# Kernel optimization log

Measured on AMD Instinct MI355X. Metric: run time of the kernel, lower is better.

## Reference

```python
import jax, jax.numpy as jnp
import numpy as np

B, T, D = 2, 2048, 1024
H, DK, DV, NH = 8, 128, 256, 2  # heads, key dim, value dim (expand_v=2), num_householder
CONV = 4
INTER = 2816
EPS = 1e-6


def rmsnorm(x, w):
    return x * jax.lax.rsqrt(jnp.mean(x * x, -1, keepdims=True) + EPS) * w


def l2norm(x):
    return x * jax.lax.rsqrt(jnp.sum(x * x, -1, keepdims=True) + 1e-6)


def causal_conv_silu(x, w):
    # depthwise causal conv1d with silu activation; x: [B,T,C], w: [C,K]
    K = w.shape[1]
    xp = jnp.pad(x, ((0, 0), (K - 1, 0), (0, 0)))
    y = sum(xp[:, i:i + x.shape[1], :] * w[:, i] for i in range(K))
    return jax.nn.silu(y)


def setup_inputs():
    key = jax.random.key(0)
    ks = jax.random.split(key, 16)
    s = 0.02
    return {
        "hidden_states": jax.random.normal(ks[0], (B, T, D), jnp.float32),
        "attn_norm_w": jnp.ones((D,), jnp.float32),
        "Wq": jax.random.normal(ks[1], (D, H * DK), jnp.float32) * s,
        "Wk": jax.random.normal(ks[2], (D, NH * H * DK), jnp.float32) * s,
        "Wv": jax.random.normal(ks[3], (D, NH * H * DV), jnp.float32) * s,
        "Wb": jax.random.normal(ks[4], (D, H * NH), jnp.float32) * s,
        "Wa": jax.random.normal(ks[5], (D, H), jnp.float32) * s,
        "A_log": jnp.log(jax.random.uniform(ks[6], (H,), jnp.float32, 1.0, 16.0)),
        "dt_bias": jax.random.normal(ks[7], (H,), jnp.float32) * 0.5,
        "conv_q_w": jax.random.normal(ks[8], (H * DK, CONV), jnp.float32) * 0.5,
        "conv_k_w": jax.random.normal(ks[9], (NH * H * DK, CONV), jnp.float32) * 0.5,
        "conv_v_w": jax.random.normal(ks[10], (NH * H * DV, CONV), jnp.float32) * 0.5,
        "Wg": jax.random.normal(ks[11], (D, H * DV), jnp.float32) * s,
        "o_norm_w": jnp.ones((DV,), jnp.float32),
        "Wo": jax.random.normal(ks[12], (H * DV, D), jnp.float32) * s,
        "mlp_norm_w": jnp.ones((D,), jnp.float32),
        "Wgate": jax.random.normal(ks[13], (D, 2 * INTER), jnp.float32) * s,
        "Wdown": jax.random.normal(ks[14], (INTER, D), jnp.float32) * s,
    }


def reference(hidden_states, attn_norm_w, Wq, Wk, Wv, Wb, Wa, A_log, dt_bias,
              conv_q_w, conv_k_w, conv_v_w, Wg, o_norm_w, Wo,
              mlp_norm_w, Wgate, Wdown):
    residual = hidden_states
    x = rmsnorm(hidden_states, attn_norm_w)

    # projections + short conv + silu, then L2-normalized q/k (gated delta rule)
    q = l2norm(causal_conv_silu(x @ Wq, conv_q_w).reshape(B, T, H, DK))
    k = l2norm(causal_conv_silu(x @ Wk, conv_k_w).reshape(B, T, NH, H, DK))
    v = causal_conv_silu(x @ Wv, conv_v_w).reshape(B, T, NH, H, DV)
    beta = jax.nn.sigmoid(x @ Wb).reshape(B, T, H, NH)
    g = -jnp.exp(A_log) * jax.nn.softplus(x @ Wa + dt_bias)  # [B,T,H] log-decay

    def step(S, inp):
        q_t, k_t, v_t, b_t, g_t = inp
        # forget gate applied once per token, then NH Householder delta-rule updates
        S = S * jnp.exp(g_t)[..., None, None]  # S: [B,H,DK,DV]
        for j in range(NH):
            kj, vj, bj = k_t[:, j], v_t[:, j], b_t[..., j]
            kS = jnp.einsum('bhk,bhkv->bhv', kj, S)
            S = S + bj[..., None, None] * jnp.einsum('bhk,bhv->bhkv', kj, vj - kS)
        o_t = jnp.einsum('bhk,bhkv->bhv', q_t, S)
        return S, o_t

    S0 = jnp.zeros((B, H, DK, DV), x.dtype)
    xs = (jnp.swapaxes(q, 0, 1), jnp.swapaxes(k, 0, 1), jnp.swapaxes(v, 0, 1),
          jnp.swapaxes(beta, 0, 1), jnp.swapaxes(g, 0, 1))
    _, o = jax.lax.scan(step, S0, xs)  # [T,B,H,DV]
    o = jnp.swapaxes(o, 0, 1)

    # gated RMSNorm output gate + output projection
    gate = (x @ Wg).reshape(B, T, H, DV)
    o = rmsnorm(o, o_norm_w) * jax.nn.silu(gate)
    hidden = residual + o.reshape(B, T, H * DV) @ Wo

    # GatedMLP (swiglu)
    y = rmsnorm(hidden, mlp_norm_w)
    gate_m, up = jnp.split(y @ Wgate, 2, -1)
    return hidden + (jax.nn.silu(gate_m) * up) @ Wdown
```

## Files before the change

kernel.cpp:

```cpp
#include <hip/hip_runtime.h>
#include <hip/hip_bf16.h>
#include <math.h>

#define Bq 2
#define Tq 2048
#define Dq 1024
#define Hq 8
#define DKq 128
#define DVq 256
#define NHq 2
#define BTq (Bq*Tq)
#define INTERq 2816

typedef __hip_bfloat16 bf16;
typedef short bfv8 __attribute__((ext_vector_type(8)));
typedef float f32v4 __attribute__((ext_vector_type(4)));

__device__ __forceinline__ float b2f(bf16 v){ return __bfloat162float(v); }
__device__ __forceinline__ bf16 f2b(float v){ return __float2bfloat16(v); }

__device__ __forceinline__ int is_f32(const unsigned* magic){ return magic[0] == 0x3F800000u; }

__device__ __forceinline__ float ldin(const void* p, int f32, size_t i){
  return f32 ? ((const float*)p)[i] : b2f(((const bf16*)p)[i]);
}

__device__ __forceinline__ float block_reduce_sum(float v, float* red){
  #pragma unroll
  for (int off = 32; off > 0; off >>= 1) v += __shfl_down(v, off, 64);
  int lane = threadIdx.x & 63, wid = threadIdx.x >> 6;
  if (lane == 0) red[wid] = v;
  __syncthreads();
  int nw = (blockDim.x + 63) >> 6;
  float tot = 0.f;
  for (int i = 0; i < nw; i++) tot += red[i];
  return tot;
}

__global__ __launch_bounds__(256) void rmsnorm_kernel(const void* __restrict__ in, int in_mode,
    const void* __restrict__ w, const unsigned* __restrict__ magic,
    bf16* __restrict__ out){
  __shared__ float red[4];
  int f32 = is_f32(magic);
  int inf32 = in_mode ? 1 : f32;
  size_t row = blockIdx.x;
  float xv[4];
  float ss = 0.f;
  #pragma unroll
  for (int j = 0; j < 4; j++){
    int i = threadIdx.x + j*256;
    float v = ldin(in, inf32, row*Dq + i);
    xv[j] = v; ss += v*v;
  }
  float tot = block_reduce_sum(ss, red);
  float sc = rsqrtf(tot / (float)Dq + 1e-6f);
  #pragma unroll
  for (int j = 0; j < 4; j++){
    int i = threadIdx.x + j*256;
    out[row*Dq + i] = f2b(xv[j] * sc * ldin(w, f32, i));
  }
}

__global__ __launch_bounds__(256) void wsplit_kernel(
    const void* __restrict__ W, const unsigned* __restrict__ magic,
    bf16* __restrict__ hi, bf16* __restrict__ lo, int K, int N){
  __shared__ float tile[32][33];
  int f32 = is_f32(magic);
  int n0 = blockIdx.x * 32, k0 = blockIdx.y * 32;
  int tx = threadIdx.x & 31, ty = threadIdx.x >> 5;
  #pragma unroll
  for (int r = 0; r < 4; r++){
    int kr = ty + r*8;
    tile[kr][tx] = ldin(W, f32, (size_t)(k0 + kr)*N + n0 + tx);
  }
  __syncthreads();
  #pragma unroll
  for (int r = 0; r < 4; r++){
    int nr = ty + r*8;
    float v = tile[tx][nr];
    bf16 h = f2b(v);
    size_t idx = (size_t)(n0 + nr)*K + k0 + tx;
    hi[idx] = h;
    if (f32) lo[idx] = f2b(v - b2f(h));
  }
}

__global__ __launch_bounds__(256) void gemm_mfma_kernel(
    const bf16* __restrict__ A, const bf16* __restrict__ WThi, const bf16* __restrict__ WTlo,
    const unsigned* __restrict__ magic,
    const void* __restrict__ res, int res_mode,
    void* __restrict__ out, int out_mode,
    int M, int N, int K){
  int f32 = is_f32(magic);
  int tid = threadIdx.x;
  int lane = tid & 63, w = tid >> 6;
  int wm = w >> 1, wn = w & 1;
  int l15 = lane & 15, quad = lane >> 4;
  size_t bm = (size_t)blockIdx.x * 128, bn = (size_t)blockIdx.y * 128;

  f32v4 acc[4][4];
  #pragma unroll
  for (int mt = 0; mt < 4; mt++)
    #pragma unroll
    for (int nt = 0; nt < 4; nt++) acc[mt][nt] = 0.f;

  const bf16* Ab = A    + (bm + wm*64 + l15)*(size_t)K + quad*8;
  const bf16* Bh = WThi + (bn + wn*64 + l15)*(size_t)K + quad*8;
  const bf16* Bl = WTlo + (bn + wn*64 + l15)*(size_t)K + quad*8;

  if (f32){
    for (int k0 = 0; k0 < K; k0 += 32){
      bfv8 a[4];
      #pragma unroll
      for (int mt = 0; mt < 4; mt++)
        a[mt] = *(const bfv8*)(Ab + (size_t)mt*16*K + k0);
      #pragma unroll
      for (int nt = 0; nt < 4; nt++){
        bfv8 bh = *(const bfv8*)(Bh + (size_t)nt*16*K + k0);
        bfv8 bl = *(const bfv8*)(Bl + (size_t)nt*16*K + k0);
        #pragma unroll
        for (int mt = 0; mt < 4; mt++){
          acc[mt][nt] = __builtin_amdgcn_mfma_f32_16x16x32_bf16(a[mt], bh, acc[mt][nt], 0, 0, 0);
          acc[mt][nt] = __builtin_amdgcn_mfma_f32_16x16x32_bf16(a[mt], bl, acc[mt][nt], 0, 0, 0);
        }
      }
    }
  } else {
    for (int k0 = 0; k0 < K; k0 += 32){
      bfv8 a[4];
      #pragma unroll
      for (int mt = 0; mt < 4; mt++)
        a[mt] = *(const bfv8*)(Ab + (size_t)mt*16*K + k0);
      #pragma unroll
      for (int nt = 0; nt < 4; nt++){
        bfv8 bh = *(const bfv8*)(Bh + (size_t)nt*16*K + k0);
        #pragma unroll
        for (int mt = 0; mt < 4; mt++)
          acc[mt][nt] = __builtin_amdgcn_mfma_f32_16x16x32_bf16(a[mt], bh, acc[mt][nt], 0, 0, 0);
      }
    }
  }
  #pragma unroll
  for (int mt = 0; mt < 4; mt++)
    #pragma unroll
    for (int nt = 0; nt < 4; nt++)
      #pragma unroll
      for (int r = 0; r < 4; r++){
        size_t row = bm + wm*64 + mt*16 + quad*4 + r;
        size_t col = bn + wn*64 + nt*16 + l15;
        float v = acc[mt][nt][r];
        if (res_mode == 1) v += ldin(res, f32, row*N + col);
        else if (res_mode == 2) v += ((const float*)res)[row*N + col];
        if (out_mode == 0) ((float*)out)[row*N + col] = v;
        else if (out_mode == 1) ((bf16*)out)[row*N + col] = f2b(v);
        else { if (f32) ((float*)out)[row*N + col] = v; else ((bf16*)out)[row*N + col] = f2b(v); }
      }
}

__global__ __launch_bounds__(256) void betag_kernel(
    const bf16* __restrict__ x, const void* __restrict__ Wb, const void* __restrict__ Wa,
    const void* __restrict__ A_log, const void* __restrict__ dt_bias,
    const unsigned* __restrict__ magic,
    float* __restrict__ beta, float* __restrict__ g){
  __shared__ float xs[Dq];
  int f32 = is_f32(magic);
  size_t bt = blockIdx.x;
  for (int i = threadIdx.x; i < Dq; i += 256) xs[i] = b2f(x[bt*Dq + i]);
  __syncthreads();
  int n = threadIdx.x;
  if (n < 16){
    float a = 0.f;
    for (int i = 0; i < Dq; i++) a = fmaf(xs[i], ldin(Wb, f32, (size_t)i*16 + n), a);
    int h = n >> 1, j = n & 1;
    beta[(bt*Hq + h)*NHq + j] = 1.f / (1.f + expf(-a));
  } else if (n < 24){
    int h = n - 16;
    float a = 0.f;
    for (int i = 0; i < Dq; i++) a = fmaf(xs[i], ldin(Wa, f32, (size_t)i*Hq + h), a);
    a += ldin(dt_bias, f32, h);
    float sp = (a > 20.f) ? a : log1pf(expf(a));
    g[bt*Hq + h] = -expf(ldin(A_log, f32, h)) * sp;
  }
}

__global__ __launch_bounds__(128) void conv_silu_kernel(
    const bf16* __restrict__ in, const void* __restrict__ w,
    const unsigned* __restrict__ magic,
    float* __restrict__ out, int C){
  __shared__ float red[2];
  int f32 = is_f32(magic);
  int bt = blockIdx.x;
  int t = bt & (Tq - 1);
  int c = blockIdx.y * 128 + threadIdx.x;
  float acc = 0.f;
  #pragma unroll
  for (int i = 0; i < 4; i++){
    int tt = t - 3 + i;
    if (tt >= 0) acc = fmaf(b2f(in[(size_t)(bt - 3 + i)*C + c]), ldin(w, f32, (size_t)c*4 + i), acc);
  }
  float y = acc / (1.f + expf(-acc));
  float tot = block_reduce_sum(y*y, red);
  y *= rsqrtf(tot + 1e-6f);
  out[(size_t)bt*C + c] = y;
}

#define DPP_ADD(x, ctrl) ((x) + __int_as_float(__builtin_amdgcn_update_dpp( \
    0, __float_as_int(x), (ctrl), 0xF, 0xF, true)))
#define KRED(p) { p = DPP_ADD(p, 0x128); p = DPP_ADD(p, 0x124); \
                  p = DPP_ADD(p, 0x122); p = DPP_ADD(p, 0x121); }

__global__ __launch_bounds__(64, 1) void scan_kernel(
    const float* __restrict__ qn,
    const float* __restrict__ kn,
    const bf16*  __restrict__ vpre,
    const void* __restrict__ conv_v, const unsigned* __restrict__ magic,
    const float* __restrict__ beta,
    const float* __restrict__ g,
    float* __restrict__ o){
  int f32 = is_f32(magic);
  int bh = blockIdx.x;
  int b = bh >> 3, h = bh & 7;
  int lane = threadIdx.x;
  int kg = lane & 15;
  int vloc = lane >> 4;
  int vv = blockIdx.y * 4 + vloc;
  int c0 = (h << 8) + vv;
  int c1 = ((Hq + h) << 8) + vv;
  float wv00 = ldin(conv_v, f32, (size_t)c0*4 + 0);
  float wv01 = ldin(conv_v, f32, (size_t)c0*4 + 1);
  float wv02 = ldin(conv_v, f32, (size_t)c0*4 + 2);
  float wv03 = ldin(conv_v, f32, (size_t)c0*4 + 3);
  float wv10 = ldin(conv_v, f32, (size_t)c1*4 + 0);
  float wv11 = ldin(conv_v, f32, (size_t)c1*4 + 1);
  float wv12 = ldin(conv_v, f32, (size_t)c1*4 + 2);
  float wv13 = ldin(conv_v, f32, (size_t)c1*4 + 3);
  const size_t base = (size_t)b * Tq;
  const float* knh = kn + base*2048 + h*DKq + kg*8;
  const float* qnh = qn + (base*Hq + h)*(size_t)DKq + kg*8;
  const bf16*  vph = vpre + base*4096;
  const float* gh  = g + base*Hq + h;
  const float2* bph = (const float2*)(beta + (base*Hq + h)*(size_t)NHq);
  float* oh = o + (base*Hq + h)*(size_t)DVq + vv;

  float4 S0 = {0,0,0,0}, S1 = {0,0,0,0};
#define SDOT(Ka, Kb, p) { \
    float e0 = fmaf(Ka.x, S0.x, Ka.y * S0.y); \
    float e1 = fmaf(Ka.z, S0.z, Ka.w * S0.w); \
    float e2 = fmaf(Kb.x, S1.x, Kb.y * S1.y); \
    float e3 = fmaf(Kb.z, S1.z, Kb.w * S1.w); \
    p = (e0 + e1) + (e2 + e3); }
#define SUPD(Ka, Kb, d) { \
    S0.x = fmaf(Ka.x, d, S0.x); S0.y = fmaf(Ka.y, d, S0.y); \
    S0.z = fmaf(Ka.z, d, S0.z); S0.w = fmaf(Ka.w, d, S0.w); \
    S1.x = fmaf(Kb.x, d, S1.x); S1.y = fmaf(Kb.y, d, S1.y); \
    S1.z = fmaf(Kb.z, d, S1.z); S1.w = fmaf(Kb.w, d, S1.w); }

  float r0a = 0.f, r1a = 0.f, r2a = 0.f;
  float r0b = 0.f, r1b = 0.f, r2b = 0.f;

  float4 A0E = *(const float4*)(knh);
  float4 A1E = *(const float4*)(knh + 4);
  float4 B0E = *(const float4*)(knh + 1024);
  float4 B1E = *(const float4*)(knh + 1028);
  float4 Q0E = *(const float4*)(qnh);
  float4 Q1E = *(const float4*)(qnh + 4);
  float4 A0O = *(const float4*)(knh + 2048);
  float4 A1O = *(const float4*)(knh + 2052);
  float4 B0O = *(const float4*)(knh + 3072);
  float4 B1O = *(const float4*)(knh + 3076);
  float4 Q0O = *(const float4*)(qnh + 1024);
  float4 Q1O = *(const float4*)(qnh + 1028);
  float  gE  = gh[0],   gO  = gh[8];
  float2 beE = bph[0],  beO = bph[8];
  float vaE = b2f(vph[c0]),        vbE = b2f(vph[c1]);
  float vaO = b2f(vph[4096 + c0]), vbO = b2f(vph[4096 + c1]);

#define STEP(A0,A1,B0,B1,Q0,Q1, gS, beS, vaS, vbS, t, tp) { \
    float eg = __expf(gS); \
    gS = gh[(tp)*8]; \
    S0.x *= eg; S0.y *= eg; S0.z *= eg; S0.w *= eg; \
    S1.x *= eg; S1.y *= eg; S1.z *= eg; S1.w *= eg; \
     \
    { float p; SDOT(A0, A1, p) \
      KRED(p) \
      float vacc = fmaf(r0a, wv00, fmaf(r1a, wv01, fmaf(r2a, wv02, vaS*wv03))); \
      float vj = vacc * __builtin_amdgcn_rcpf(1.f + __expf(-vacc)); \
      float delta = beS.x * (vj - p); \
      SUPD(A0, A1, delta) \
      A0 = *(const float4*)(knh + (tp)*2048); \
      A1 = *(const float4*)(knh + (tp)*2048 + 4); \
      r0a = r1a; r1a = r2a; r2a = vaS; \
      vaS = b2f(vph[(tp)*4096 + c0]); } \
     \
    { float p; SDOT(B0, B1, p) \
      KRED(p) \
      float vacc = fmaf(r0b, wv10, fmaf(r1b, wv11, fmaf(r2b, wv12, vbS*wv13))); \
      float vj = vacc * __builtin_amdgcn_rcpf(1.f + __expf(-vacc)); \
      float delta = beS.y * (vj - p); \
      SUPD(B0, B1, delta) \
      B0 = *(const float4*)(knh + (tp)*2048 + 1024); \
      B1 = *(const float4*)(knh + (tp)*2048 + 1028); \
      r0b = r1b; r1b = r2b; r2b = vbS; \
      vbS = b2f(vph[(tp)*4096 + c1]); } \
    beS = bph[(tp)*8]; \
     \
     \
    { float p; SDOT(Q0, Q1, p) \
      KRED(p) \
      oh[(t)*2048] = p; \
      Q0 = *(const float4*)(qnh + (tp)*1024); \
      Q1 = *(const float4*)(qnh + (tp)*1024 + 4); } \
    __builtin_amdgcn_sched_barrier(0); }

  for (int t = 0; t < Tq; t += 2){
    STEP(A0E,A1E,B0E,B1E,Q0E,Q1E, gE,beE,vaE,vbE, t,   t+2)
    STEP(A0O,A1O,B0O,B1O,Q0O,Q1O, gO,beO,vaO,vbO, t+1, t+3)
  }
#undef STEP
#undef SDOT
#undef SUPD
}

__global__ __launch_bounds__(256) void gate_o_kernel(
    const float* __restrict__ o, const void* __restrict__ onw,
    const unsigned* __restrict__ magic,
    const bf16* __restrict__ gate, bf16* __restrict__ og){
  __shared__ float red[4];
  int f32 = is_f32(magic);
  size_t bth = blockIdx.x;
  int dv = threadIdx.x;
  float v = o[bth*DVq + dv];
  float tot = block_reduce_sum(v*v, red);
  float sc = rsqrtf(tot / (float)DVq + 1e-6f);
  float gt = b2f(gate[bth*DVq + dv]);
  float silu = gt / (1.f + expf(-gt));
  og[bth*DVq + dv] = f2b(v * sc * ldin(onw, f32, dv) * silu);
}

__global__ __launch_bounds__(256) void silumul_kernel(
    const bf16* __restrict__ gu, bf16* __restrict__ mid, int n){
  int i = blockIdx.x * 256 + threadIdx.x;
  if (i >= n) return;
  int bt = i / INTERq, c = i % INTERq;
  float gm = b2f(gu[(size_t)bt*2*INTERq + c]);
  float up = b2f(gu[(size_t)bt*2*INTERq + INTERq + c]);
  mid[i] = f2b(gm / (1.f + expf(-gm)) * up);
}

extern "C" void kernel_launch(void* const* d_in, const int* in_sizes, int n_in,
                              void* d_out, int out_size, void* d_ws, size_t ws_size,
                              hipStream_t stream){
  const void* hs      = d_in[0];
  const unsigned* magic = (const unsigned*)d_in[1];
  const void* attn_nw = d_in[1];
  const void* Wq      = d_in[2];
  const void* Wk      = d_in[3];
  const void* Wv      = d_in[4];
  const void* Wb      = d_in[5];
  const void* Wa      = d_in[6];
  const void* A_log   = d_in[7];
  const void* dt_bias = d_in[8];
  const void* conv_q  = d_in[9];
  const void* conv_k  = d_in[10];
  const void* conv_v  = d_in[11];
  const void* Wg      = d_in[12];
  const void* o_nw    = d_in[13];
  const void* Wo      = d_in[14];
  const void* mlp_nw  = d_in[15];
  const void* Wgate   = d_in[16];
  const void* Wdown   = d_in[17];

  char* ws = (char*)d_ws;
  const size_t MB = (size_t)1 << 20;
  size_t X     = 0;
  size_t QPRE  = 8*MB;
  size_t KPRE  = 16*MB;
  size_t VPRE  = 32*MB;
  size_t GATE  = 64*MB;
  size_t QN    = 80*MB;
  size_t KN    = 96*MB;
  size_t HID   = 128*MB;
  size_t BETA  = 144*MB;
  size_t Gb    = 144*MB + 512*1024;
  size_t O      = 0;
  size_t OG     = QN;
  size_t Y      = KN;
  size_t GATEUP = 0;
  size_t MID    = 44*MB;
  size_t W0 = 145*MB;
  size_t WTQh = W0 +  0*MB, WTQl = W0 +  2*MB;
  size_t WTKh = W0 +  4*MB, WTKl = W0 +  8*MB;
  size_t WTVh = W0 + 12*MB, WTVl = W0 + 20*MB;
  size_t WTGh = W0 + 28*MB, WTGl = W0 + 32*MB;
  size_t WTOh = W0 + 36*MB, WTOl = W0 + 40*MB;
  size_t WTUh = W0 + 44*MB, WTUl = W0 + 56*MB;
  size_t WTDh = W0 + 68*MB, WTDl = W0 + 74*MB;
  (void)ws_size; (void)in_sizes; (void)n_in; (void)out_size;

  wsplit_kernel<<<dim3(1024/32, 1024/32), 256, 0, stream>>>(Wq,    magic, (bf16*)(ws+WTQh), (bf16*)(ws+WTQl), 1024, 1024);
  wsplit_kernel<<<dim3(2048/32, 1024/32), 256, 0, stream>>>(Wk,    magic, (bf16*)(ws+WTKh), (bf16*)(ws+WTKl), 1024, 2048);
  wsplit_kernel<<<dim3(4096/32, 1024/32), 256, 0, stream>>>(Wv,    magic, (bf16*)(ws+WTVh), (bf16*)(ws+WTVl), 1024, 4096);
  wsplit_kernel<<<dim3(2048/32, 1024/32), 256, 0, stream>>>(Wg,    magic, (bf16*)(ws+WTGh), (bf16*)(ws+WTGl), 1024, 2048);
  wsplit_kernel<<<dim3(1024/32, 2048/32), 256, 0, stream>>>(Wo,    magic, (bf16*)(ws+WTOh), (bf16*)(ws+WTOl), 2048, 1024);
  wsplit_kernel<<<dim3(5632/32, 1024/32), 256, 0, stream>>>(Wgate, magic, (bf16*)(ws+WTUh), (bf16*)(ws+WTUl), 1024, 5632);
  wsplit_kernel<<<dim3(1024/32, 2816/32), 256, 0, stream>>>(Wdown, magic, (bf16*)(ws+WTDh), (bf16*)(ws+WTDl), 2816, 1024);

  rmsnorm_kernel<<<BTq, 256, 0, stream>>>(hs, 0, attn_nw, magic, (bf16*)(ws+X));

  gemm_mfma_kernel<<<dim3(32,  8), 256, 0, stream>>>((bf16*)(ws+X), (bf16*)(ws+WTQh), (bf16*)(ws+WTQl), magic, nullptr, 0, ws+QPRE, 1, BTq, 1024, 1024);
  gemm_mfma_kernel<<<dim3(32, 16), 256, 0, stream>>>((bf16*)(ws+X), (bf16*)(ws+WTKh), (bf16*)(ws+WTKl), magic, nullptr, 0, ws+KPRE, 1, BTq, 2048, 1024);
  gemm_mfma_kernel<<<dim3(32, 32), 256, 0, stream>>>((bf16*)(ws+X), (bf16*)(ws+WTVh), (bf16*)(ws+WTVl), magic, nullptr, 0, ws+VPRE, 1, BTq, 4096, 1024);
  gemm_mfma_kernel<<<dim3(32, 16), 256, 0, stream>>>((bf16*)(ws+X), (bf16*)(ws+WTGh), (bf16*)(ws+WTGl), magic, nullptr, 0, ws+GATE, 1, BTq, 2048, 1024);
  betag_kernel<<<BTq, 256, 0, stream>>>((bf16*)(ws+X), Wb, Wa, A_log, dt_bias, magic, (float*)(ws+BETA), (float*)(ws+Gb));

  conv_silu_kernel<<<dim3(BTq, 1024/128), 128, 0, stream>>>((bf16*)(ws+QPRE), conv_q, magic, (float*)(ws+QN), 1024);
  conv_silu_kernel<<<dim3(BTq, 2048/128), 128, 0, stream>>>((bf16*)(ws+KPRE), conv_k, magic, (float*)(ws+KN), 2048);

  scan_kernel<<<dim3(Bq*Hq, DVq/4), 64, 0, stream>>>(
      (const float*)(ws+QN), (const float*)(ws+KN), (const bf16*)(ws+VPRE),
      conv_v, magic, (const float*)(ws+BETA), (const float*)(ws+Gb), (float*)(ws+O));

  gate_o_kernel<<<BTq*Hq, 256, 0, stream>>>((const float*)(ws+O), o_nw, magic, (const bf16*)(ws+GATE), (bf16*)(ws+OG));

  gemm_mfma_kernel<<<dim3(32, 8), 256, 0, stream>>>((bf16*)(ws+OG), (bf16*)(ws+WTOh), (bf16*)(ws+WTOl), magic, hs, 1, ws+HID, 0, BTq, 1024, 2048);

  rmsnorm_kernel<<<BTq, 256, 0, stream>>>(ws+HID, 1, mlp_nw, magic, (bf16*)(ws+Y));

  gemm_mfma_kernel<<<dim3(32, 44), 256, 0, stream>>>((bf16*)(ws+Y), (bf16*)(ws+WTUh), (bf16*)(ws+WTUl), magic, nullptr, 0, ws+GATEUP, 1, BTq, 5632, 1024);

  int nmid = BTq * INTERq;
  silumul_kernel<<<(nmid + 255)/256, 256, 0, stream>>>((const bf16*)(ws+GATEUP), (bf16*)(ws+MID), nmid);

  gemm_mfma_kernel<<<dim3(32, 8), 256, 0, stream>>>((bf16*)(ws+MID), (bf16*)(ws+WTDh), (bf16*)(ws+WTDl), magic, ws+HID, 2, d_out, 2, BTq, 1024, 2816);
}
```

Measured before the change: 2.652 ms.

## Hoist v conv+silu and decay exp out of scan; parallelize beta/g reduction

Moves the causal conv + SiLU on v out of the serial scan into a separate parallel kernel that writes bf16, and precomputes exp(g) in the beta/g kernel so the scan only multiplies. The beta/g kernel now spreads each dot product over a full wavefront with a shuffle reduction instead of one thread per output. The scan's output store is also limited to one lane per 16-lane group instead of all lanes. This shortens the latency-bound per-token critical path, at the cost of an extra kernel launch and an extra bf16 write and read of v.

```diff
diff --git a/kernel.cpp b/kernel.cpp
--- a/kernel.cpp
+++ b/kernel.cpp
@@ -161,25 +161,44 @@
     const bf16* __restrict__ x, const void* __restrict__ Wb, const void* __restrict__ Wa,
     const void* __restrict__ A_log, const void* __restrict__ dt_bias,
     const unsigned* __restrict__ magic,
-    float* __restrict__ beta, float* __restrict__ g){
+    float* __restrict__ beta, float* __restrict__ eg){
   __shared__ float xs[Dq];
   int f32 = is_f32(magic);
   size_t bt = blockIdx.x;
   for (int i = threadIdx.x; i < Dq; i += 256) xs[i] = b2f(x[bt*Dq + i]);
   __syncthreads();
-  int n = threadIdx.x;
-  if (n < 16){
+  int wv = threadIdx.x >> 6, lane = threadIdx.x & 63;
+  #pragma unroll
+  for (int r = 0; r < 6; r++){
+    int n = wv*6 + r;
     float a = 0.f;
-    for (int i = 0; i < Dq; i++) a = fmaf(xs[i], ldin(Wb, f32, (size_t)i*16 + n), a);
-    int h = n >> 1, j = n & 1;
-    beta[(bt*Hq + h)*NHq + j] = 1.f / (1.f + expf(-a));
-  } else if (n < 24){
-    int h = n - 16;
-    float a = 0.f;
-    for (int i = 0; i < Dq; i++) a = fmaf(xs[i], ldin(Wa, f32, (size_t)i*Hq + h), a);
-    a += ldin(dt_bias, f32, h);
-    float sp = (a > 20.f) ? a : log1pf(expf(a));
-    g[bt*Hq + h] = -expf(ldin(A_log, f32, h)) * sp;
+    if (n < 16){
+      #pragma unroll
+      for (int e = 0; e < 16; e++){
+        int i = lane + 64*e;
+        a = fmaf(xs[i], ldin(Wb, f32, (size_t)i*16 + n), a);
+      }
+    } else {
+      int h = n - 16;
+      #pragma unroll
+      for (int e = 0; e < 16; e++){
+        int i = lane + 64*e;
+        a = fmaf(xs[i], ldin(Wa, f32, (size_t)i*8 + h), a);
+      }
+    }
+    #pragma unroll
+    for (int off = 32; off > 0; off >>= 1) a += __shfl_down(a, off, 64);
+    if (lane == 0){
+      if (n < 16){
+        int h = n >> 1, j = n & 1;
+        beta[(bt*Hq + h)*NHq + j] = 1.f / (1.f + expf(-a));
+      } else {
+        int h = n - 16;
+        a += ldin(dt_bias, f32, h);
+        float sp = (a > 20.f) ? a : log1pf(expf(a));
+        eg[bt*Hq + h] = expf(-expf(ldin(A_log, f32, h)) * sp);
+      }
+    }
   }
 }
 
@@ -204,6 +223,22 @@
   out[(size_t)bt*C + c] = y;
 }
 
+__global__ __launch_bounds__(256) void conv_v_kernel(
+    const bf16* __restrict__ in, const void* __restrict__ w,
+    const unsigned* __restrict__ magic, bf16* __restrict__ out){
+  int f32 = is_f32(magic);
+  int bt = blockIdx.x;
+  int t = bt & (Tq - 1);
+  int c = blockIdx.y * 256 + threadIdx.x;
+  float acc = 0.f;
+  #pragma unroll
+  for (int i = 0; i < 4; i++){
+    int tt = t - 3 + i;
+    if (tt >= 0) acc = fmaf(b2f(in[(size_t)(bt - 3 + i)*4096 + c]), ldin(w, f32, (size_t)c*4 + i), acc);
+  }
+  out[(size_t)bt*4096 + c] = f2b(acc / (1.f + expf(-acc)));
+}
+
 #define DPP_ADD(x, ctrl) ((x) + __int_as_float(__builtin_amdgcn_update_dpp( \
     0, __float_as_int(x), (ctrl), 0xF, 0xF, true)))
 #define KRED(p) { p = DPP_ADD(p, 0x128); p = DPP_ADD(p, 0x124); \
@@ -212,12 +247,10 @@
 __global__ __launch_bounds__(64, 1) void scan_kernel(
     const float* __restrict__ qn,
     const float* __restrict__ kn,
-    const bf16*  __restrict__ vpre,
-    const void* __restrict__ conv_v, const unsigned* __restrict__ magic,
+    const bf16*  __restrict__ vcv,
     const float* __restrict__ beta,
-    const float* __restrict__ g,
+    const float* __restrict__ eg,
     float* __restrict__ o){
-  int f32 = is_f32(magic);
   int bh = blockIdx.x;
   int b = bh >> 3, h = bh & 7;
   int lane = threadIdx.x;
@@ -225,20 +258,12 @@
   int vloc = lane >> 4;
   int vv = blockIdx.y * 4 + vloc;
   int c0 = (h << 8) + vv;
-  int c1 = ((Hq + h) << 8) + vv;
-  float wv00 = ldin(conv_v, f32, (size_t)c0*4 + 0);
-  float wv01 = ldin(conv_v, f32, (size_t)c0*4 + 1);
-  float wv02 = ldin(conv_v, f32, (size_t)c0*4 + 2);
-  float wv03 = ldin(conv_v, f32, (size_t)c0*4 + 3);
-  float wv10 = ldin(conv_v, f32, (size_t)c1*4 + 0);
-  float wv11 = ldin(conv_v, f32, (size_t)c1*4 + 1);
-  float wv12 = ldin(conv_v, f32, (size_t)c1*4 + 2);
-  float wv13 = ldin(conv_v, f32, (size_t)c1*4 + 3);
+  int c1 = 2048 + (h << 8) + vv;
   const size_t base = (size_t)b * Tq;
   const float* knh = kn + base*2048 + h*DKq + kg*8;
   const float* qnh = qn + (base*Hq + h)*(size_t)DKq + kg*8;
-  const bf16*  vph = vpre + base*4096;
-  const float* gh  = g + base*Hq + h;
+  const bf16*  vph = vcv + base*4096;
+  const float* gh  = eg + base*Hq + h;
   const float2* bph = (const float2*)(beta + (base*Hq + h)*(size_t)NHq);
   float* oh = o + (base*Hq + h)*(size_t)DVq + vv;
 
@@ -254,9 +279,6 @@
     S0.z = fmaf(Ka.z, d, S0.z); S0.w = fmaf(Ka.w, d, S0.w); \
     S1.x = fmaf(Kb.x, d, S1.x); S1.y = fmaf(Kb.y, d, S1.y); \
     S1.z = fmaf(Kb.z, d, S1.z); S1.w = fmaf(Kb.w, d, S1.w); }
-
-  float r0a = 0.f, r1a = 0.f, r2a = 0.f;
-  float r0b = 0.f, r1b = 0.f, r2b = 0.f;
 
   float4 A0E = *(const float4*)(knh);
   float4 A1E = *(const float4*)(knh + 4);
@@ -276,38 +298,31 @@
   float vaO = b2f(vph[4096 + c0]), vbO = b2f(vph[4096 + c1]);
 
 #define STEP(A0,A1,B0,B1,Q0,Q1, gS, beS, vaS, vbS, t, tp) { \
-    float eg = __expf(gS); \
+    float egv = gS; \
     gS = gh[(tp)*8]; \
-    S0.x *= eg; S0.y *= eg; S0.z *= eg; S0.w *= eg; \
-    S1.x *= eg; S1.y *= eg; S1.z *= eg; S1.w *= eg; \
+    S0.x *= egv; S0.y *= egv; S0.z *= egv; S0.w *= egv; \
+    S1.x *= egv; S1.y *= egv; S1.z *= egv; S1.w *= egv; \
      \
     { float p; SDOT(A0, A1, p) \
       KRED(p) \
-      float vacc = fmaf(r0a, wv00, fmaf(r1a, wv01, fmaf(r2a, wv02, vaS*wv03))); \
-      float vj = vacc * __builtin_amdgcn_rcpf(1.f + __expf(-vacc)); \
-      float delta = beS.x * (vj - p); \
+      float delta = beS.x * (vaS - p); \
       SUPD(A0, A1, delta) \
       A0 = *(const float4*)(knh + (tp)*2048); \
       A1 = *(const float4*)(knh + (tp)*2048 + 4); \
-      r0a = r1a; r1a = r2a; r2a = vaS; \
       vaS = b2f(vph[(tp)*4096 + c0]); } \
      \
     { float p; SDOT(B0, B1, p) \
       KRED(p) \
-      float vacc = fmaf(r0b, wv10, fmaf(r1b, wv11, fmaf(r2b, wv12, vbS*wv13))); \
-      float vj = vacc * __builtin_amdgcn_rcpf(1.f + __expf(-vacc)); \
-      float delta = beS.y * (vj - p); \
+      float delta = beS.y * (vbS - p); \
       SUPD(B0, B1, delta) \
       B0 = *(const float4*)(knh + (tp)*2048 + 1024); \
       B1 = *(const float4*)(knh + (tp)*2048 + 1028); \
-      r0b = r1b; r1b = r2b; r2b = vbS; \
       vbS = b2f(vph[(tp)*4096 + c1]); } \
     beS = bph[(tp)*8]; \
      \
-     \
     { float p; SDOT(Q0, Q1, p) \
       KRED(p) \
-      oh[(t)*2048] = p; \
+      if ((lane & 15) == 0) oh[(t)*2048] = p; \
       Q0 = *(const float4*)(qnh + (tp)*1024); \
       Q1 = *(const float4*)(qnh + (tp)*1024 + 4); } \
     __builtin_amdgcn_sched_barrier(0); }
@@ -382,7 +397,8 @@
   size_t HID   = 128*MB;
   size_t BETA  = 144*MB;
   size_t Gb    = 144*MB + 512*1024;
-  size_t O      = 0;
+  size_t VCV    = 0;
+  size_t O      = 32*MB;
   size_t OG     = QN;
   size_t Y      = KN;
   size_t GATEUP = 0;
@@ -415,10 +431,11 @@
 
   conv_silu_kernel<<<dim3(BTq, 1024/128), 128, 0, stream>>>((bf16*)(ws+QPRE), conv_q, magic, (float*)(ws+QN), 1024);
   conv_silu_kernel<<<dim3(BTq, 2048/128), 128, 0, stream>>>((bf16*)(ws+KPRE), conv_k, magic, (float*)(ws+KN), 2048);
+  conv_v_kernel<<<dim3(BTq, 4096/256), 256, 0, stream>>>((bf16*)(ws+VPRE), conv_v, magic, (bf16*)(ws+VCV));
 
   scan_kernel<<<dim3(Bq*Hq, DVq/4), 64, 0, stream>>>(
-      (const float*)(ws+QN), (const float*)(ws+KN), (const bf16*)(ws+VPRE),
-      conv_v, magic, (const float*)(ws+BETA), (const float*)(ws+Gb), (float*)(ws+O));
+      (const float*)(ws+QN), (const float*)(ws+KN), (const bf16*)(ws+VCV),
+      (const float*)(ws+BETA), (const float*)(ws+Gb), (float*)(ws+O));
 
   gate_o_kernel<<<BTq*Hq, 256, 0, stream>>>((const float*)(ws+O), o_nw, magic, (const bf16*)(ws+GATE), (bf16*)(ws+OG));
 
```

Result: faster. 2.441 ms (-7.9%).
